# Performance work log

Hardware: AMD Instinct MI355X
Metric: run time of the kernel (lower is better)

## Reference

```python
import jax, jax.numpy as jnp
import numpy as np

N_NODES = 50000
D = 128
BN_EPS = 1e-5
GIN_EPS = 0.0  # GINConv default eps


def setup_inputs() -> dict:
    key = jax.random.key(0)
    ks = jax.random.split(key, 8)
    feature = jax.random.normal(ks[0], (N_NODES, D), dtype=jnp.float32)
    edge_index = jax.random.randint(ks[1], (2, 600000), 0, N_NODES, dtype=jnp.int32)
    s = 1.0 / np.sqrt(D)
    W1 = jax.random.uniform(ks[2], (D, D), jnp.float32, -s, s)
    b1 = jax.random.uniform(ks[3], (D,), jnp.float32, -s, s)
    W2 = jax.random.uniform(ks[4], (D, D), jnp.float32, -s, s)
    b2 = jax.random.uniform(ks[5], (D,), jnp.float32, -s, s)
    gamma = jnp.ones((D,), jnp.float32)
    beta = jnp.zeros((D,), jnp.float32)
    return {"feature": feature, "edge_index": edge_index,
            "W1": W1, "b1": b1, "W2": W2, "b2": b2,
            "gamma": gamma, "beta": beta}


def reference(feature, edge_index, W1, b1, W2, b2, gamma, beta):
    src, dst = edge_index[0], edge_index[1]
    # GIN aggregation: sum of neighbor (source) features at each target node
    agg = jax.ops.segment_sum(feature[src], dst, num_segments=N_NODES)
    h = (1.0 + GIN_EPS) * feature + agg
    # 2-layer MLP
    h = jax.nn.relu(h @ W1 + b1) @ W2 + b2
    # outer ReLU
    y = jax.nn.relu(h)
    # BatchNorm1d (training mode: batch statistics, biased variance)
    mean = jnp.mean(y, axis=0)
    var = jnp.mean(jnp.square(y - mean), axis=0)
    out = (y - mean) * jax.lax.rsqrt(var + BN_EPS) * gamma + beta
    return out
```

## Files before the change

### kernel.cpp

```cpp
#include <hip/hip_runtime.h>

#define N_NODES 50000
#define D 128
#define N_EDGES 600000
#define BN_EPS 1e-5f
#define NREP 8
#define BUCKET 64

#define MLP_BLOCKS 512
#define MLP_WAVES  (MLP_BLOCKS * 4)
#define N_GROUPS   3125

#define NBINS   196
#define BINCAP  4096
#define SA_EPB  2048
#define SA_BLOCKS 293

#define FEATC_BLOCKS 3125
#define WPREP_BLOCKS 128
#define ZERO_BLOCKS  9

typedef __attribute__((ext_vector_type(8))) short short8;
typedef __attribute__((ext_vector_type(4))) float floatx4;

__device__ __forceinline__ unsigned f2bf(float f) {
    unsigned x = __float_as_uint(f);
    return (x + 0x7fffu + ((x >> 16) & 1u)) >> 16;
}
__device__ __forceinline__ float bflo(unsigned v) { return __uint_as_float(v << 16); }
__device__ __forceinline__ float bfhi(unsigned v) { return __uint_as_float(v & 0xffff0000u); }

__global__ void prep_kernel(const float* __restrict__ f, unsigned* __restrict__ fb,
                            const float* __restrict__ W1, const float* __restrict__ W2,
                            unsigned short* __restrict__ Wt1, unsigned short* __restrict__ Wt2,
                            float* __restrict__ stats) {
    int b = blockIdx.x;
    int tid = threadIdx.x;
    if (b < FEATC_BLOCKS) {
        int gid = b * 256 + tid;
        float4 a = ((const float4*)f)[gid * 2];
        float4 c = ((const float4*)f)[gid * 2 + 1];
        uint4 o;
        o.x = f2bf(a.x) | (f2bf(a.y) << 16);
        o.y = f2bf(a.z) | (f2bf(a.w) << 16);
        o.z = f2bf(c.x) | (f2bf(c.y) << 16);
        o.w = f2bf(c.z) | (f2bf(c.w) << 16);
        ((uint4*)fb)[gid] = o;
    } else if (b < FEATC_BLOCKS + WPREP_BLOCKS) {
        int gid = (b - FEATC_BLOCKS) * 256 + tid;
        int m = gid >> 14;
        int idx = gid & (D * D - 1);
        int k = idx >> 7;
        int n = idx & 127;
        const float* W = m ? W2 : W1;
        unsigned short* Wt = m ? Wt2 : Wt1;
        Wt[n * D + k] = (unsigned short)f2bf(W[k * D + n]);
    } else {
        int sid = (b - FEATC_BLOCKS - WPREP_BLOCKS) * 256 + tid;
        if (sid < NREP * 256 + 256) stats[sid] = 0.f;
    }
}

__global__ __launch_bounds__(256) void bin_scatter_a(const int* __restrict__ ei,
                                                     int* __restrict__ binCnt,
                                                     unsigned* __restrict__ binBuf) {
    __shared__ int hist[NBINS];
    __shared__ int base[NBINS];
    const int tid = threadIdx.x;
    for (int i = tid; i < NBINS; i += 256) hist[i] = 0;
    __syncthreads();

    const int e0 = blockIdx.x * SA_EPB;
    const int nE = min(SA_EPB, N_EDGES - e0);

    unsigned pk[8];
    int lp[8];
    int bn_[8];
    #pragma unroll
    for (int k = 0; k < 8; ++k) {
        int idx = tid + k * 256;
        if (idx < nE) {
            int e = e0 + idx;
            unsigned src = (unsigned)ei[e];
            unsigned dst = (unsigned)ei[N_EDGES + e];
            int bb = (int)(dst >> 8);
            pk[k] = (dst << 16) | src;
            bn_[k] = bb;
            lp[k] = atomicAdd(&hist[bb], 1);
        } else {
            bn_[k] = -1;
        }
    }
    __syncthreads();
    for (int bb = tid; bb < NBINS; bb += 256) {
        int h = hist[bb];
        base[bb] = h ? atomicAdd(&binCnt[bb], h) : 0;
    }
    __syncthreads();
    #pragma unroll
    for (int k = 0; k < 8; ++k) {
        if (bn_[k] >= 0)
            binBuf[bn_[k] * BINCAP + base[bn_[k]] + lp[k]] = pk[k];
    }
}

__global__ __launch_bounds__(1024) void bin_scatter_b(const unsigned* __restrict__ binBuf,
                                                      const int* __restrict__ binCnt,
                                                      int* __restrict__ cnt,
                                                      unsigned short* __restrict__ ssrc) {
    __shared__ int lcnt[256];
    const int tid = threadIdx.x;
    const int b = blockIdx.x;
    if (tid < 256) lcnt[tid] = 0;
    __syncthreads();

    const int E = binCnt[b];
    const unsigned* buf = binBuf + b * BINCAP;
    for (int i = tid; i < E; i += 1024) {
        unsigned p = buf[i];
        int dst = (int)(p >> 16);
        int src = (int)(p & 0xffffu);
        int pos = atomicAdd(&lcnt[dst & 255], 1);
        ssrc[dst * BUCKET + pos] = (unsigned short)src;
    }
    __syncthreads();
    const int n0 = b << 8;
    if (tid < 256 && n0 + tid < N_NODES) cnt[n0 + tid] = lcnt[tid];
}

__global__ __launch_bounds__(256) void gather_kernel(const uint4* __restrict__ fb4,
                                                     const int* __restrict__ cnt,
                                                     const unsigned short* __restrict__ ssrc,
                                                     uint4* __restrict__ hb4) {
    int wave = (blockIdx.x * 256 + threadIdx.x) >> 6;
    int lane = threadIdx.x & 63;
    int quad = lane >> 4;
    int l16 = lane & 15;
    int node = wave * 4 + quad;
    int beg = node * BUCKET;
    int end = beg + cnt[node];

    uint4 own = fb4[node * 16 + l16];
    float a0 = bflo(own.x), a1 = bfhi(own.x);
    float a2 = bflo(own.y), a3 = bfhi(own.y);
    float a4 = bflo(own.z), a5 = bfhi(own.z);
    float a6 = bflo(own.w), a7 = bfhi(own.w);

    int j = beg;
    #define ACC8(v) do { \
        a0 += bflo((v).x); a1 += bfhi((v).x); \
        a2 += bflo((v).y); a3 += bfhi((v).y); \
        a4 += bflo((v).z); a5 += bfhi((v).z); \
        a6 += bflo((v).w); a7 += bfhi((v).w); } while (0)
    for (; j + 7 < end; j += 8) {
        uint4 sv = *(const uint4*)&ssrc[j];
        int i0 = sv.x & 0xffff, i1 = sv.x >> 16;
        int i2 = sv.y & 0xffff, i3 = sv.y >> 16;
        int i4 = sv.z & 0xffff, i5 = sv.z >> 16;
        int i6 = sv.w & 0xffff, i7 = sv.w >> 16;
        uint4 v0 = fb4[i0 * 16 + l16];
        uint4 v1 = fb4[i1 * 16 + l16];
        uint4 v2 = fb4[i2 * 16 + l16];
        uint4 v3 = fb4[i3 * 16 + l16];
        uint4 v4 = fb4[i4 * 16 + l16];
        uint4 v5 = fb4[i5 * 16 + l16];
        uint4 v6 = fb4[i6 * 16 + l16];
        uint4 v7 = fb4[i7 * 16 + l16];
        ACC8(v0); ACC8(v1); ACC8(v2); ACC8(v3);
        ACC8(v4); ACC8(v5); ACC8(v6); ACC8(v7);
    }
    if (j + 3 < end) {
        ushort4 sv = *(const ushort4*)&ssrc[j];
        uint4 v0 = fb4[(int)sv.x * 16 + l16];
        uint4 v1 = fb4[(int)sv.y * 16 + l16];
        uint4 v2 = fb4[(int)sv.z * 16 + l16];
        uint4 v3 = fb4[(int)sv.w * 16 + l16];
        ACC8(v0); ACC8(v1); ACC8(v2); ACC8(v3);
        j += 4;
    }
    for (; j < end; ++j) {
        uint4 v = fb4[(int)ssrc[j] * 16 + l16];
        ACC8(v);
    }
    #undef ACC8

    uint4 o;
    o.x = f2bf(a0) | (f2bf(a1) << 16);
    o.y = f2bf(a2) | (f2bf(a3) << 16);
    o.z = f2bf(a4) | (f2bf(a5) << 16);
    o.w = f2bf(a6) | (f2bf(a7) << 16);
    hb4[node * 16 + l16] = o;
}

__global__ __launch_bounds__(256) void mlp_kernel(
    const unsigned short* __restrict__ A,
    const unsigned short* __restrict__ Bt1, const unsigned short* __restrict__ Bt2,
    const float* __restrict__ bias1, const float* __restrict__ bias2,
    unsigned short* __restrict__ yb, float* __restrict__ stats)
{
    __shared__ unsigned short B1lds[128 * 128];
    __shared__ unsigned short B2lds[128 * 128];
    __shared__ unsigned short Xch[4 * 16 * 128];

    const int tid = threadIdx.x;

    #pragma unroll
    for (int i = 0; i < 8; ++i) {
        int c = tid + i * 256;
        int row = c >> 4;
        int g = c & 15;
        int dst = row * 128 + (g ^ (row & 15)) * 8;
        int src = row * 128 + g * 8;
        *(uint4*)&B1lds[dst] = *(const uint4*)&Bt1[src];
        *(uint4*)&B2lds[dst] = *(const uint4*)&Bt2[src];
    }
    __syncthreads();

    const int lane = tid & 63;
    const int wid = tid >> 6;
    const int l15 = lane & 15;
    const int quad = lane >> 4;
    unsigned short* X = &Xch[wid * 2048];

    float bs1[8], bs2[8];
    #pragma unroll
    for (int n = 0; n < 8; ++n) {
        bs1[n] = bias1[n * 16 + l15];
        bs2[n] = bias2[n * 16 + l15];
    }

    float s[8], q[8];
    #pragma unroll
    for (int n = 0; n < 8; ++n) { s[n] = 0.f; q[n] = 0.f; }

    const int gw = blockIdx.x * 4 + wid;
    const int g1 = gw + MLP_WAVES;
    const bool has1 = (g1 < N_GROUPS);

    short8 afA[4], afB[4];
    #pragma unroll
    for (int kc = 0; kc < 4; ++kc)
        afA[kc] = *(const short8*)&A[(gw * 16 + l15) * 128 + kc * 32 + quad * 8];
    if (has1) {
        #pragma unroll
        for (int kc = 0; kc < 4; ++kc)
            afB[kc] = *(const short8*)&A[(g1 * 16 + l15) * 128 + kc * 32 + quad * 8];
    }

    auto compute = [&](int rowBase, short8* af) {
        floatx4 acc[8];
        #pragma unroll
        for (int n = 0; n < 8; ++n) acc[n] = (floatx4){0.f, 0.f, 0.f, 0.f};
        #pragma unroll
        for (int kc = 0; kc < 4; ++kc) {
            int ga = (kc * 4 + quad) ^ l15;
            #pragma unroll
            for (int n = 0; n < 8; ++n) {
                short8 bf = *(const short8*)&B1lds[(n * 16 + l15) * 128 + ga * 8];
                acc[n] = __builtin_amdgcn_mfma_f32_16x16x32_bf16(af[kc], bf, acc[n], 0, 0, 0);
            }
        }

        #pragma unroll
        for (int n = 0; n < 8; ++n) {
            int col = n * 16 + l15;
            int gg = col >> 3;
            int o7 = col & 7;
            #pragma unroll
            for (int r = 0; r < 4; ++r) {
                int rl = quad * 4 + r;
                float v = fmaxf(acc[n][r] + bs1[n], 0.f);
                X[rl * 128 + ((gg ^ rl) * 8) + o7] = (unsigned short)f2bf(v);
            }
        }
        short8 hf[4];
        #pragma unroll
        for (int kc = 0; kc < 4; ++kc)
            hf[kc] = *(const short8*)&X[l15 * 128 + (((kc * 4 + quad) ^ l15) * 8)];

        #pragma unroll
        for (int n = 0; n < 8; ++n) acc[n] = (floatx4){0.f, 0.f, 0.f, 0.f};
        #pragma unroll
        for (int kc = 0; kc < 4; ++kc) {
            int ga = (kc * 4 + quad) ^ l15;
            #pragma unroll
            for (int n = 0; n < 8; ++n) {
                short8 bf = *(const short8*)&B2lds[(n * 16 + l15) * 128 + ga * 8];
                acc[n] = __builtin_amdgcn_mfma_f32_16x16x32_bf16(hf[kc], bf, acc[n], 0, 0, 0);
            }
        }

        #pragma unroll
        for (int n = 0; n < 8; ++n) {
            int col = n * 16 + l15;
            #pragma unroll
            for (int r = 0; r < 4; ++r) {
                int row = rowBase + quad * 4 + r;
                float v = fmaxf(acc[n][r] + bs2[n], 0.f);
                yb[row * 128 + col] = (unsigned short)f2bf(v);
                s[n] += v;
                q[n] += v * v;
            }
        }
    };

    compute(gw * 16, afA);
    if (has1) compute(g1 * 16, afB);

    #pragma unroll
    for (int n = 0; n < 8; ++n) {
        s[n] += __shfl_xor(s[n], 16);
        s[n] += __shfl_xor(s[n], 32);
        q[n] += __shfl_xor(q[n], 16);
        q[n] += __shfl_xor(q[n], 32);
    }
    __syncthreads();
    float* red = (float*)B1lds;
    if (lane < 16) {
        #pragma unroll
        for (int n = 0; n < 8; ++n) {
            red[wid * 128 + n * 16 + lane] = s[n];
            red[512 + wid * 128 + n * 16 + lane] = q[n];
        }
    }
    __syncthreads();
    float* myStats = stats + (blockIdx.x & (NREP - 1)) * 256;
    if (tid < 128) {
        float ss = 0.f, qq = 0.f;
        #pragma unroll
        for (int w = 0; w < 4; ++w) {
            ss += red[w * 128 + tid];
            qq += red[512 + w * 128 + tid];
        }
        atomicAdd(&myStats[tid], ss);
        atomicAdd(&myStats[128 + tid], qq);
    }
}

__global__ __launch_bounds__(256) void bn_kernel(const uint4* __restrict__ yb4,
                                                 float* __restrict__ out,
                                                 const float* __restrict__ stats,
                                                 const float* __restrict__ gamma,
                                                 const float* __restrict__ beta)
{
    __shared__ float red[256];
    __shared__ float sc[128], sh[128];
    int tid = threadIdx.x;

    float acc = 0.f;
    #pragma unroll
    for (int r = 0; r < NREP; ++r) acc += stats[r * 256 + tid];
    red[tid] = acc;
    __syncthreads();
    if (tid < 128) {
        const float inv_n = 1.0f / (float)N_NODES;
        float m = red[tid] * inv_n;
        float var = red[128 + tid] * inv_n - m * m;
        float scale = gamma[tid] * rsqrtf(var + BN_EPS);
        sc[tid] = scale;
        sh[tid] = beta[tid] - m * scale;
    }
    __syncthreads();

    const int n8 = N_NODES * D / 8;
    int base = (blockIdx.x * 256 + tid) * 4;
    #pragma unroll
    for (int i = 0; i < 4; ++i) {
        int idx = base + i;
        if (idx >= n8) break;
        int c0 = (idx << 3) & 127;
        uint4 v = yb4[idx];
        float4 o0, o1;
        o0.x = bflo(v.x) * sc[c0 + 0] + sh[c0 + 0];
        o0.y = bfhi(v.x) * sc[c0 + 1] + sh[c0 + 1];
        o0.z = bflo(v.y) * sc[c0 + 2] + sh[c0 + 2];
        o0.w = bfhi(v.y) * sc[c0 + 3] + sh[c0 + 3];
        o1.x = bflo(v.z) * sc[c0 + 4] + sh[c0 + 4];
        o1.y = bfhi(v.z) * sc[c0 + 5] + sh[c0 + 5];
        o1.z = bflo(v.w) * sc[c0 + 6] + sh[c0 + 6];
        o1.w = bfhi(v.w) * sc[c0 + 7] + sh[c0 + 7];
        ((float4*)out)[idx * 2] = o0;
        ((float4*)out)[idx * 2 + 1] = o1;
    }
}

extern "C" void kernel_launch(void* const* d_in, const int* in_sizes, int n_in,
                              void* d_out, int out_size, void* d_ws, size_t ws_size,
                              hipStream_t stream) {
    const float* feature = (const float*)d_in[0];
    const int*   ei      = (const int*)d_in[1];
    const float* W1      = (const float*)d_in[2];
    const float* b1      = (const float*)d_in[3];
    const float* W2      = (const float*)d_in[4];
    const float* b2      = (const float*)d_in[5];
    const float* gamma   = (const float*)d_in[6];
    const float* beta    = (const float*)d_in[7];
    float* out = (float*)d_out;

    unsigned*       featb  = (unsigned*)d_ws;
    unsigned*       hb     = featb + N_NODES * 64;
    unsigned*       yb32   = hb + N_NODES * 64;
    unsigned short* Wt1    = (unsigned short*)(yb32 + N_NODES * 64);
    unsigned short* Wt2    = Wt1 + D * D;
    float*          stats  = (float*)(Wt2 + D * D);
    int*            binCnt = (int*)(stats + NREP * 256);
    int*            cnt    = binCnt + 256;
    unsigned short* ssrc   = (unsigned short*)(cnt + N_NODES);
    unsigned*       binBuf = (unsigned*)(ssrc + N_NODES * BUCKET);
    unsigned short* yb     = (unsigned short*)yb32;

    prep_kernel<<<FEATC_BLOCKS + WPREP_BLOCKS + ZERO_BLOCKS, 256, 0, stream>>>(
        feature, featb, W1, W2, Wt1, Wt2, stats);
    bin_scatter_a<<<SA_BLOCKS, 256, 0, stream>>>(ei, binCnt, binBuf);
    bin_scatter_b<<<NBINS, 1024, 0, stream>>>(binBuf, binCnt, cnt, ssrc);
    gather_kernel<<<N_NODES / 4 * 64 / 256, 256, 0, stream>>>(
        (const uint4*)featb, cnt, ssrc, (uint4*)hb);
    mlp_kernel<<<MLP_BLOCKS, 256, 0, stream>>>(
        (const unsigned short*)hb, Wt1, Wt2, b1, b2, yb, stats);
    bn_kernel<<<(N_NODES * D / 8 / 4 + 255) / 256, 256, 0, stream>>>(
        (const uint4*)yb, out, stats, gamma, beta);
}
```

Before: 157.7 us.

## Sort nodes by degree for gather balance and interleave two MLP tiles

bin_scatter_b now builds a per-bin counting sort of nodes by in-degree and emits a packed (node, degree) order list. The gather kernel uses that list so each wave processes nodes of similar degree, which cuts divergence among the four quads that share a wave. The MLP kernel runs both row groups' MFMA chains together instead of one after the other, which adds independent matrix work to hide MFMA latency at the cost of more registers. It also clamps bucket overflow past 64 neighbours.

New measurement: 161.7 us. 1.03x slower.

```diff
diff --git a/kernel.cpp b/kernel.cpp
--- a/kernel.cpp
+++ b/kernel.cpp
@@ -106,12 +106,14 @@
 
 __global__ __launch_bounds__(1024) void bin_scatter_b(const unsigned* __restrict__ binBuf,
                                                       const int* __restrict__ binCnt,
-                                                      int* __restrict__ cnt,
+                                                      unsigned* __restrict__ nodeOrd,
                                                       unsigned short* __restrict__ ssrc) {
     __shared__ int lcnt[256];
+    __shared__ int dhist[BUCKET + 1];
     const int tid = threadIdx.x;
     const int b = blockIdx.x;
     if (tid < 256) lcnt[tid] = 0;
+    if (tid >= 256 && tid < 256 + BUCKET + 1) dhist[tid - 256] = 0;
     __syncthreads();
 
     const int E = binCnt[b];
@@ -121,24 +123,43 @@
         int dst = (int)(p >> 16);
         int src = (int)(p & 0xffffu);
         int pos = atomicAdd(&lcnt[dst & 255], 1);
-        ssrc[dst * BUCKET + pos] = (unsigned short)src;
-    }
-    __syncthreads();
+        if (pos < BUCKET) ssrc[dst * BUCKET + pos] = (unsigned short)src;
+    }
+    __syncthreads();
+
     const int n0 = b << 8;
-    if (tid < 256 && n0 + tid < N_NODES) cnt[n0 + tid] = lcnt[tid];
+    const int nIn = min(256, N_NODES - n0);
+    int deg = 0;
+    if (tid < nIn) {
+        deg = min(lcnt[tid], BUCKET);
+        atomicAdd(&dhist[deg], 1);
+    }
+    __syncthreads();
+    if (tid == 0) {
+        int acc = 0;
+        #pragma unroll
+        for (int d = 0; d <= BUCKET; ++d) { int h = dhist[d]; dhist[d] = acc; acc += h; }
+    }
+    __syncthreads();
+    if (tid < nIn) {
+        int r = atomicAdd(&dhist[deg], 1);
+        nodeOrd[n0 + r] = ((unsigned)(n0 + tid) << 8) | (unsigned)deg;
+    }
 }
 
 __global__ __launch_bounds__(256) void gather_kernel(const uint4* __restrict__ fb4,
-                                                     const int* __restrict__ cnt,
+                                                     const unsigned* __restrict__ nodeOrd,
                                                      const unsigned short* __restrict__ ssrc,
                                                      uint4* __restrict__ hb4) {
     int wave = (blockIdx.x * 256 + threadIdx.x) >> 6;
     int lane = threadIdx.x & 63;
     int quad = lane >> 4;
     int l16 = lane & 15;
-    int node = wave * 4 + quad;
+    unsigned pk = nodeOrd[wave * 4 + quad];
+    int node = (int)(pk >> 8);
+    int deg = (int)(pk & 255u);
     int beg = node * BUCKET;
-    int end = beg + cnt[node];
+    int end = beg + deg;
 
     uint4 own = fb4[node * 16 + l16];
     float a0 = bflo(own.x), a1 = bfhi(own.x);
@@ -236,76 +257,104 @@
     const int gw = blockIdx.x * 4 + wid;
     const int g1 = gw + MLP_WAVES;
     const bool has1 = (g1 < N_GROUPS);
+    const int g1m = has1 ? g1 : gw;
 
     short8 afA[4], afB[4];
     #pragma unroll
     for (int kc = 0; kc < 4; ++kc)
         afA[kc] = *(const short8*)&A[(gw * 16 + l15) * 128 + kc * 32 + quad * 8];
-    if (has1) {
-        #pragma unroll
-        for (int kc = 0; kc < 4; ++kc)
-            afB[kc] = *(const short8*)&A[(g1 * 16 + l15) * 128 + kc * 32 + quad * 8];
-    }
-
-    auto compute = [&](int rowBase, short8* af) {
-        floatx4 acc[8];
-        #pragma unroll
-        for (int n = 0; n < 8; ++n) acc[n] = (floatx4){0.f, 0.f, 0.f, 0.f};
-        #pragma unroll
-        for (int kc = 0; kc < 4; ++kc) {
-            int ga = (kc * 4 + quad) ^ l15;
-            #pragma unroll
-            for (int n = 0; n < 8; ++n) {
-                short8 bf = *(const short8*)&B1lds[(n * 16 + l15) * 128 + ga * 8];
-                acc[n] = __builtin_amdgcn_mfma_f32_16x16x32_bf16(af[kc], bf, acc[n], 0, 0, 0);
-            }
-        }
-
+    #pragma unroll
+    for (int kc = 0; kc < 4; ++kc)
+        afB[kc] = *(const short8*)&A[(g1m * 16 + l15) * 128 + kc * 32 + quad * 8];
+
+    floatx4 aA[8], aB[8];
+    #pragma unroll
+    for (int n = 0; n < 8; ++n) { aA[n] = (floatx4){0.f,0.f,0.f,0.f}; aB[n] = (floatx4){0.f,0.f,0.f,0.f}; }
+    #pragma unroll
+    for (int kc = 0; kc < 4; ++kc) {
+        int ga = (kc * 4 + quad) ^ l15;
         #pragma unroll
         for (int n = 0; n < 8; ++n) {
-            int col = n * 16 + l15;
-            int gg = col >> 3;
-            int o7 = col & 7;
-            #pragma unroll
-            for (int r = 0; r < 4; ++r) {
-                int rl = quad * 4 + r;
-                float v = fmaxf(acc[n][r] + bs1[n], 0.f);
-                X[rl * 128 + ((gg ^ rl) * 8) + o7] = (unsigned short)f2bf(v);
-            }
-        }
-        short8 hf[4];
-        #pragma unroll
-        for (int kc = 0; kc < 4; ++kc)
-            hf[kc] = *(const short8*)&X[l15 * 128 + (((kc * 4 + quad) ^ l15) * 8)];
-
-        #pragma unroll
-        for (int n = 0; n < 8; ++n) acc[n] = (floatx4){0.f, 0.f, 0.f, 0.f};
-        #pragma unroll
-        for (int kc = 0; kc < 4; ++kc) {
-            int ga = (kc * 4 + quad) ^ l15;
-            #pragma unroll
-            for (int n = 0; n < 8; ++n) {
-                short8 bf = *(const short8*)&B2lds[(n * 16 + l15) * 128 + ga * 8];
-                acc[n] = __builtin_amdgcn_mfma_f32_16x16x32_bf16(hf[kc], bf, acc[n], 0, 0, 0);
-            }
-        }
-
+            short8 bf = *(const short8*)&B1lds[(n * 16 + l15) * 128 + ga * 8];
+            aA[n] = __builtin_amdgcn_mfma_f32_16x16x32_bf16(afA[kc], bf, aA[n], 0, 0, 0);
+            aB[n] = __builtin_amdgcn_mfma_f32_16x16x32_bf16(afB[kc], bf, aB[n], 0, 0, 0);
+        }
+    }
+
+    #pragma unroll
+    for (int n = 0; n < 8; ++n) {
+        int col = n * 16 + l15;
+        int gg = col >> 3;
+        int o7 = col & 7;
+        #pragma unroll
+        for (int r = 0; r < 4; ++r) {
+            int rl = quad * 4 + r;
+            float v = fmaxf(aA[n][r] + bs1[n], 0.f);
+            X[rl * 128 + ((gg ^ rl) * 8) + o7] = (unsigned short)f2bf(v);
+        }
+    }
+    #pragma unroll
+    for (int kc = 0; kc < 4; ++kc)
+        afA[kc] = *(const short8*)&X[l15 * 128 + (((kc * 4 + quad) ^ l15) * 8)];
+    #pragma unroll
+    for (int n = 0; n < 8; ++n) {
+        int col = n * 16 + l15;
+        int gg = col >> 3;
+        int o7 = col & 7;
+        #pragma unroll
+        for (int r = 0; r < 4; ++r) {
+            int rl = quad * 4 + r;
+            float v = fmaxf(aB[n][r] + bs1[n], 0.f);
+            X[rl * 128 + ((gg ^ rl) * 8) + o7] = (unsigned short)f2bf(v);
+        }
+    }
+    #pragma unroll
+    for (int kc = 0; kc < 4; ++kc)
+        afB[kc] = *(const short8*)&X[l15 * 128 + (((kc * 4 + quad) ^ l15) * 8)];
+
+    #pragma unroll
+    for (int n = 0; n < 8; ++n) { aA[n] = (floatx4){0.f,0.f,0.f,0.f}; aB[n] = (floatx4){0.f,0.f,0.f,0.f}; }
+    #pragma unroll
+    for (int kc = 0; kc < 4; ++kc) {
+        int ga = (kc * 4 + quad) ^ l15;
+        #pragma unroll
+        for (int n = 0; n < 8; ++n) {
+            short8 bf = *(const short8*)&B2lds[(n * 16 + l15) * 128 + ga * 8];
+            aA[n] = __builtin_amdgcn_mfma_f32_16x16x32_bf16(afA[kc], bf, aA[n], 0, 0, 0);
+            aB[n] = __builtin_amdgcn_mfma_f32_16x16x32_bf16(afB[kc], bf, aB[n], 0, 0, 0);
+        }
+    }
+
+    {
+        const int rowBase = gw * 16;
         #pragma unroll
         for (int n = 0; n < 8; ++n) {
             int col = n * 16 + l15;
             #pragma unroll
             for (int r = 0; r < 4; ++r) {
                 int row = rowBase + quad * 4 + r;
-                float v = fmaxf(acc[n][r] + bs2[n], 0.f);
+                float v = fmaxf(aA[n][r] + bs2[n], 0.f);
                 yb[row * 128 + col] = (unsigned short)f2bf(v);
                 s[n] += v;
                 q[n] += v * v;
             }
         }
-    };
-
-    compute(gw * 16, afA);
-    if (has1) compute(g1 * 16, afB);
+    }
+    if (has1) {
+        const int rowBase = g1 * 16;
+        #pragma unroll
+        for (int n = 0; n < 8; ++n) {
+            int col = n * 16 + l15;
+            #pragma unroll
+            for (int r = 0; r < 4; ++r) {
+                int row = rowBase + quad * 4 + r;
+                float v = fmaxf(aB[n][r] + bs2[n], 0.f);
+                yb[row * 128 + col] = (unsigned short)f2bf(v);
+                s[n] += v;
+                q[n] += v * v;
+            }
+        }
+    }
 
     #pragma unroll
     for (int n = 0; n < 8; ++n) {
@@ -397,24 +446,24 @@
     const float* beta    = (const float*)d_in[7];
     float* out = (float*)d_out;
 
-    unsigned*       featb  = (unsigned*)d_ws;
-    unsigned*       hb     = featb + N_NODES * 64;
-    unsigned*       yb32   = hb + N_NODES * 64;
-    unsigned short* Wt1    = (unsigned short*)(yb32 + N_NODES * 64);
-    unsigned short* Wt2    = Wt1 + D * D;
-    float*          stats  = (float*)(Wt2 + D * D);
-    int*            binCnt = (int*)(stats + NREP * 256);
-    int*            cnt    = binCnt + 256;
-    unsigned short* ssrc   = (unsigned short*)(cnt + N_NODES);
-    unsigned*       binBuf = (unsigned*)(ssrc + N_NODES * BUCKET);
-    unsigned short* yb     = (unsigned short*)yb32;
+    unsigned*       featb   = (unsigned*)d_ws;
+    unsigned*       hb      = featb + N_NODES * 64;
+    unsigned*       yb32    = hb + N_NODES * 64;
+    unsigned short* Wt1     = (unsigned short*)(yb32 + N_NODES * 64);
+    unsigned short* Wt2     = Wt1 + D * D;
+    float*          stats   = (float*)(Wt2 + D * D);
+    int*            binCnt  = (int*)(stats + NREP * 256);
+    unsigned*       nodeOrd = (unsigned*)(binCnt + 256);
+    unsigned short* ssrc    = (unsigned short*)(nodeOrd + N_NODES);
+    unsigned*       binBuf  = (unsigned*)(ssrc + N_NODES * BUCKET);
+    unsigned short* yb      = (unsigned short*)yb32;
 
     prep_kernel<<<FEATC_BLOCKS + WPREP_BLOCKS + ZERO_BLOCKS, 256, 0, stream>>>(
         feature, featb, W1, W2, Wt1, Wt2, stats);
     bin_scatter_a<<<SA_BLOCKS, 256, 0, stream>>>(ei, binCnt, binBuf);
-    bin_scatter_b<<<NBINS, 1024, 0, stream>>>(binBuf, binCnt, cnt, ssrc);
+    bin_scatter_b<<<NBINS, 1024, 0, stream>>>(binBuf, binCnt, nodeOrd, ssrc);
     gather_kernel<<<N_NODES / 4 * 64 / 256, 256, 0, stream>>>(
-        (const uint4*)featb, cnt, ssrc, (uint4*)hb);
+        (const uint4*)featb, nodeOrd, ssrc, (uint4*)hb);
     mlp_kernel<<<MLP_BLOCKS, 256, 0, stream>>>(
         (const unsigned short*)hb, Wt1, Wt2, b1, b2, yb, stats);
     bn_kernel<<<(N_NODES * D / 8 / 4 + 255) / 256, 256, 0, stream>>>(
```

## Fuse bucket scatter into gather using shared-memory per-node source lists

Applied to the files above, without the earlier changes.

Bins shrink to 64 destination nodes (782 bins). The second scatter pass and the gather kernel are merged into one kernel. Each block builds its nodes' source lists in LDS and then gathers the features directly, which removes a kernel launch and the global ssrc/cnt write and read round trip. The cost is fewer blocks (782) each handling 64 nodes serially per wave, so parallelism drops. Bins are capped (1024 edges, 64 per node), which silently drops edges if the caps overflow. The MLP's second-tile A loads are also made unconditional by clamping the group index.

New measurement: 155.3 us, median of 2. No clear change (-1.6%).

```diff
diff --git a/kernel.cpp b/kernel.cpp
--- a/kernel.cpp
+++ b/kernel.cpp
@@ -11,14 +11,14 @@
 #define MLP_WAVES  (MLP_BLOCKS * 4)
 #define N_GROUPS   3125
 
-#define NBINS   196
-#define BINCAP  4096
+#define NBINS   782
+#define BINCAP  1024
 #define SA_EPB  2048
 #define SA_BLOCKS 293
 
 #define FEATC_BLOCKS 3125
 #define WPREP_BLOCKS 128
-#define ZERO_BLOCKS  9
+#define ZERO_BLOCKS  12
 
 typedef __attribute__((ext_vector_type(8))) short short8;
 typedef __attribute__((ext_vector_type(4))) float floatx4;
@@ -57,7 +57,7 @@
         Wt[n * D + k] = (unsigned short)f2bf(W[k * D + n]);
     } else {
         int sid = (b - FEATC_BLOCKS - WPREP_BLOCKS) * 256 + tid;
-        if (sid < NREP * 256 + 256) stats[sid] = 0.f;
+        if (sid < NREP * 256 + 1024) stats[sid] = 0.f;
     }
 }
 
@@ -83,7 +83,7 @@
             int e = e0 + idx;
             unsigned src = (unsigned)ei[e];
             unsigned dst = (unsigned)ei[N_EDGES + e];
-            int bb = (int)(dst >> 8);
+            int bb = (int)(dst >> 6);
             pk[k] = (dst << 16) | src;
             bn_[k] = bb;
             lp[k] = atomicAdd(&hist[bb], 1);
@@ -99,97 +99,100 @@
     __syncthreads();
     #pragma unroll
     for (int k = 0; k < 8; ++k) {
-        if (bn_[k] >= 0)
-            binBuf[bn_[k] * BINCAP + base[bn_[k]] + lp[k]] = pk[k];
-    }
-}
-
-__global__ __launch_bounds__(1024) void bin_scatter_b(const unsigned* __restrict__ binBuf,
-                                                      const int* __restrict__ binCnt,
-                                                      int* __restrict__ cnt,
-                                                      unsigned short* __restrict__ ssrc) {
-    __shared__ int lcnt[256];
+        if (bn_[k] >= 0) {
+            int off = base[bn_[k]] + lp[k];
+            if (off < BINCAP)
+                binBuf[bn_[k] * BINCAP + off] = pk[k];
+        }
+    }
+}
+
+__global__ __launch_bounds__(256) void bucket_gather(const unsigned* __restrict__ binBuf,
+                                                     const int* __restrict__ binCnt,
+                                                     const uint4* __restrict__ fb4,
+                                                     uint4* __restrict__ hb4) {
+    __shared__ unsigned short lss[64 * BUCKET];
+    __shared__ int lcnt[64];
     const int tid = threadIdx.x;
     const int b = blockIdx.x;
-    if (tid < 256) lcnt[tid] = 0;
-    __syncthreads();
-
-    const int E = binCnt[b];
+    if (tid < 64) lcnt[tid] = 0;
+    __syncthreads();
+
+    const int E = min(binCnt[b], BINCAP);
     const unsigned* buf = binBuf + b * BINCAP;
-    for (int i = tid; i < E; i += 1024) {
+    for (int i = tid; i < E; i += 256) {
         unsigned p = buf[i];
-        int dst = (int)(p >> 16);
+        int d6 = (int)(p >> 16) & 63;
         int src = (int)(p & 0xffffu);
-        int pos = atomicAdd(&lcnt[dst & 255], 1);
-        ssrc[dst * BUCKET + pos] = (unsigned short)src;
-    }
-    __syncthreads();
-    const int n0 = b << 8;
-    if (tid < 256 && n0 + tid < N_NODES) cnt[n0 + tid] = lcnt[tid];
-}
-
-__global__ __launch_bounds__(256) void gather_kernel(const uint4* __restrict__ fb4,
-                                                     const int* __restrict__ cnt,
-                                                     const unsigned short* __restrict__ ssrc,
-                                                     uint4* __restrict__ hb4) {
-    int wave = (blockIdx.x * 256 + threadIdx.x) >> 6;
-    int lane = threadIdx.x & 63;
-    int quad = lane >> 4;
-    int l16 = lane & 15;
-    int node = wave * 4 + quad;
-    int beg = node * BUCKET;
-    int end = beg + cnt[node];
-
-    uint4 own = fb4[node * 16 + l16];
-    float a0 = bflo(own.x), a1 = bfhi(own.x);
-    float a2 = bflo(own.y), a3 = bfhi(own.y);
-    float a4 = bflo(own.z), a5 = bfhi(own.z);
-    float a6 = bflo(own.w), a7 = bfhi(own.w);
-
-    int j = beg;
-    #define ACC8(v) do { \
-        a0 += bflo((v).x); a1 += bfhi((v).x); \
-        a2 += bflo((v).y); a3 += bfhi((v).y); \
-        a4 += bflo((v).z); a5 += bfhi((v).z); \
-        a6 += bflo((v).w); a7 += bfhi((v).w); } while (0)
-    for (; j + 7 < end; j += 8) {
-        uint4 sv = *(const uint4*)&ssrc[j];
-        int i0 = sv.x & 0xffff, i1 = sv.x >> 16;
-        int i2 = sv.y & 0xffff, i3 = sv.y >> 16;
-        int i4 = sv.z & 0xffff, i5 = sv.z >> 16;
-        int i6 = sv.w & 0xffff, i7 = sv.w >> 16;
-        uint4 v0 = fb4[i0 * 16 + l16];
-        uint4 v1 = fb4[i1 * 16 + l16];
-        uint4 v2 = fb4[i2 * 16 + l16];
-        uint4 v3 = fb4[i3 * 16 + l16];
-        uint4 v4 = fb4[i4 * 16 + l16];
-        uint4 v5 = fb4[i5 * 16 + l16];
-        uint4 v6 = fb4[i6 * 16 + l16];
-        uint4 v7 = fb4[i7 * 16 + l16];
-        ACC8(v0); ACC8(v1); ACC8(v2); ACC8(v3);
-        ACC8(v4); ACC8(v5); ACC8(v6); ACC8(v7);
-    }
-    if (j + 3 < end) {
-        ushort4 sv = *(const ushort4*)&ssrc[j];
-        uint4 v0 = fb4[(int)sv.x * 16 + l16];
-        uint4 v1 = fb4[(int)sv.y * 16 + l16];
-        uint4 v2 = fb4[(int)sv.z * 16 + l16];
-        uint4 v3 = fb4[(int)sv.w * 16 + l16];
-        ACC8(v0); ACC8(v1); ACC8(v2); ACC8(v3);
-        j += 4;
-    }
-    for (; j < end; ++j) {
-        uint4 v = fb4[(int)ssrc[j] * 16 + l16];
-        ACC8(v);
-    }
-    #undef ACC8
-
-    uint4 o;
-    o.x = f2bf(a0) | (f2bf(a1) << 16);
-    o.y = f2bf(a2) | (f2bf(a3) << 16);
-    o.z = f2bf(a4) | (f2bf(a5) << 16);
-    o.w = f2bf(a6) | (f2bf(a7) << 16);
-    hb4[node * 16 + l16] = o;
+        int pos = atomicAdd(&lcnt[d6], 1);
+        if (pos < BUCKET) lss[d6 * BUCKET + pos] = (unsigned short)src;
+    }
+    __syncthreads();
+
+    const int lane = tid & 63;
+    const int wid = tid >> 6;
+    const int quad = lane >> 4;
+    const int l16 = lane & 15;
+
+    #pragma unroll
+    for (int pass = 0; pass < 4; ++pass) {
+        const int nl = pass * 16 + wid * 4 + quad;
+        const int node = (b << 6) + nl;
+        if (node >= N_NODES) continue;
+        const int deg = min(lcnt[nl], BUCKET);
+        const int lbase = nl * BUCKET;
+
+        uint4 own = fb4[node * 16 + l16];
+        float a0 = bflo(own.x), a1 = bfhi(own.x);
+        float a2 = bflo(own.y), a3 = bfhi(own.y);
+        float a4 = bflo(own.z), a5 = bfhi(own.z);
+        float a6 = bflo(own.w), a7 = bfhi(own.w);
+
+        int j = 0;
+        #define ACC8(v) do { \
+            a0 += bflo((v).x); a1 += bfhi((v).x); \
+            a2 += bflo((v).y); a3 += bfhi((v).y); \
+            a4 += bflo((v).z); a5 += bfhi((v).z); \
+            a6 += bflo((v).w); a7 += bfhi((v).w); } while (0)
+        for (; j + 7 < deg; j += 8) {
+            uint4 sv = *(const uint4*)&lss[lbase + j];
+            int i0 = sv.x & 0xffff, i1 = sv.x >> 16;
+            int i2 = sv.y & 0xffff, i3 = sv.y >> 16;
+            int i4 = sv.z & 0xffff, i5 = sv.z >> 16;
+            int i6 = sv.w & 0xffff, i7 = sv.w >> 16;
+            uint4 v0 = fb4[i0 * 16 + l16];
+            uint4 v1 = fb4[i1 * 16 + l16];
+            uint4 v2 = fb4[i2 * 16 + l16];
+            uint4 v3 = fb4[i3 * 16 + l16];
+            uint4 v4 = fb4[i4 * 16 + l16];
+            uint4 v5 = fb4[i5 * 16 + l16];
+            uint4 v6 = fb4[i6 * 16 + l16];
+            uint4 v7 = fb4[i7 * 16 + l16];
+            ACC8(v0); ACC8(v1); ACC8(v2); ACC8(v3);
+            ACC8(v4); ACC8(v5); ACC8(v6); ACC8(v7);
+        }
+        if (j + 3 < deg) {
+            ushort4 sv = *(const ushort4*)&lss[lbase + j];
+            uint4 v0 = fb4[(int)sv.x * 16 + l16];
+            uint4 v1 = fb4[(int)sv.y * 16 + l16];
+            uint4 v2 = fb4[(int)sv.z * 16 + l16];
+            uint4 v3 = fb4[(int)sv.w * 16 + l16];
+            ACC8(v0); ACC8(v1); ACC8(v2); ACC8(v3);
+            j += 4;
+        }
+        for (; j < deg; ++j) {
+            uint4 v = fb4[(int)lss[lbase + j] * 16 + l16];
+            ACC8(v);
+        }
+        #undef ACC8
+
+        uint4 o;
+        o.x = f2bf(a0) | (f2bf(a1) << 16);
+        o.y = f2bf(a2) | (f2bf(a3) << 16);
+        o.z = f2bf(a4) | (f2bf(a5) << 16);
+        o.w = f2bf(a6) | (f2bf(a7) << 16);
+        hb4[node * 16 + l16] = o;
+    }
 }
 
 __global__ __launch_bounds__(256) void mlp_kernel(
@@ -236,16 +239,15 @@
     const int gw = blockIdx.x * 4 + wid;
     const int g1 = gw + MLP_WAVES;
     const bool has1 = (g1 < N_GROUPS);
+    const int g1m = has1 ? g1 : gw;
 
     short8 afA[4], afB[4];
     #pragma unroll
     for (int kc = 0; kc < 4; ++kc)
         afA[kc] = *(const short8*)&A[(gw * 16 + l15) * 128 + kc * 32 + quad * 8];
-    if (has1) {
-        #pragma unroll
-        for (int kc = 0; kc < 4; ++kc)
-            afB[kc] = *(const short8*)&A[(g1 * 16 + l15) * 128 + kc * 32 + quad * 8];
-    }
+    #pragma unroll
+    for (int kc = 0; kc < 4; ++kc)
+        afB[kc] = *(const short8*)&A[(g1m * 16 + l15) * 128 + kc * 32 + quad * 8];
 
     auto compute = [&](int rowBase, short8* af) {
         floatx4 acc[8];
@@ -397,24 +399,21 @@
     const float* beta    = (const float*)d_in[7];
     float* out = (float*)d_out;
 
-    unsigned*       featb  = (unsigned*)d_ws;
-    unsigned*       hb     = featb + N_NODES * 64;
-    unsigned*       yb32   = hb + N_NODES * 64;
-    unsigned short* Wt1    = (unsigned short*)(yb32 + N_NODES * 64);
-    unsigned short* Wt2    = Wt1 + D * D;
-    float*          stats  = (float*)(Wt2 + D * D);
-    int*            binCnt = (int*)(stats + NREP * 256);
-    int*            cnt    = binCnt + 256;
-    unsigned short* ssrc   = (unsigned short*)(cnt + N_NODES);
-    unsigned*       binBuf = (unsigned*)(ssrc + N_NODES * BUCKET);
-    unsigned short* yb     = (unsigned short*)yb32;
+    unsigned*       featb   = (unsigned*)d_ws;
+    unsigned*       hb      = featb + N_NODES * 64;
+    unsigned*       yb32    = hb + N_NODES * 64;
+    unsigned short* Wt1     = (unsigned short*)(yb32 + N_NODES * 64);
+    unsigned short* Wt2     = Wt1 + D * D;
+    float*          stats   = (float*)(Wt2 + D * D);
+    int*            binCnt  = (int*)(stats + NREP * 256);
+    unsigned*       binBuf  = (unsigned*)(binCnt + 1024);
+    unsigned short* yb      = (unsigned short*)yb32;
 
     prep_kernel<<<FEATC_BLOCKS + WPREP_BLOCKS + ZERO_BLOCKS, 256, 0, stream>>>(
         feature, featb, W1, W2, Wt1, Wt2, stats);
     bin_scatter_a<<<SA_BLOCKS, 256, 0, stream>>>(ei, binCnt, binBuf);
-    bin_scatter_b<<<NBINS, 1024, 0, stream>>>(binBuf, binCnt, cnt, ssrc);
-    gather_kernel<<<N_NODES / 4 * 64 / 256, 256, 0, stream>>>(
-        (const uint4*)featb, cnt, ssrc, (uint4*)hb);
+    bucket_gather<<<NBINS, 256, 0, stream>>>(
+        binBuf, binCnt, (const uint4*)featb, (uint4*)hb);
     mlp_kernel<<<MLP_BLOCKS, 256, 0, stream>>>(
         (const unsigned short*)hb, Wt1, Wt2, b1, b2, yb, stats);
     bn_kernel<<<(N_NODES * D / 8 / 4 + 255) / 256, 256, 0, stream>>>(
```
